# Kernel tuning notes

Hardware: AMD Instinct MI355X
Metric: run time of the kernel (lower is better)

The kernel has to match this reference:

```python
import jax, jax.numpy as jnp
import numpy as np

B, S, HS = 2, 2048, 2048
H, KVH, D = 8, 1, 256
ROPE_BASE = 10000.0


def _rope_cos_sin(position_ids, dim, base=ROPE_BASE):
    # position_ids: (B, S) int -> cos/sin: (B, S, dim)
    inv_freq = 1.0 / (base ** (jnp.arange(0, dim, 2, dtype=jnp.float32) / dim))
    thetas = position_ids.astype(jnp.float32)[..., None] * inv_freq  # (B,S,dim/2)
    emb = jnp.concatenate([thetas, thetas], axis=-1)  # (B,S,dim)
    return jnp.cos(emb), jnp.sin(emb)


def _rotate_half(x):
    x1, x2 = jnp.split(x, 2, axis=-1)
    return jnp.concatenate([-x2, x1], axis=-1)


def _apply_rope(q, k, cos, sin):
    # q,k: (B,h,S,D); cos,sin: (B,S,D) -> unsqueeze head dim
    cos = cos[:, None, :, :]
    sin = sin[:, None, :, :]
    q_emb = q * cos + _rotate_half(q) * sin
    k_emb = k * cos + _rotate_half(k) * sin
    return q_emb, k_emb


def setup_inputs() -> dict:
    key = jax.random.key(0)
    k0, k1, k2, k3, k4 = jax.random.split(key, 5)
    hidden_states = jax.random.normal(k0, (B, S, HS), jnp.float32)
    # causal additive mask: 0 where j<=i, large negative otherwise
    causal = jnp.tril(jnp.ones((S, S), dtype=bool))
    attention_mask = jnp.where(causal, 0.0, -1e9).astype(jnp.float32)
    attention_mask = jnp.broadcast_to(attention_mask[None, None], (B, 1, S, S))
    position_ids = jnp.broadcast_to(jnp.arange(S, dtype=jnp.int32)[None], (B, S))
    scale = 0.02
    Wq = jax.random.normal(k1, (HS, H * D), jnp.float32) * scale
    Wk = jax.random.normal(k2, (HS, KVH * D), jnp.float32) * scale
    Wv = jax.random.normal(k3, (HS, KVH * D), jnp.float32) * scale
    Wo = jax.random.normal(k4, (H * D, HS), jnp.float32) * scale
    return {"hidden_states": hidden_states, "attention_mask": attention_mask,
            "position_ids": position_ids, "Wq": Wq, "Wk": Wk, "Wv": Wv, "Wo": Wo}


def reference(hidden_states, attention_mask, position_ids, Wq, Wk, Wv, Wo):
    bs, seq_len, _ = hidden_states.shape
    q = (hidden_states @ Wq).reshape(bs, seq_len, H, D).transpose(0, 2, 1, 3)     # (B,H,S,D)
    k = (hidden_states @ Wk).reshape(bs, seq_len, KVH, D).transpose(0, 2, 1, 3)   # (B,KVH,S,D)
    v = (hidden_states @ Wv).reshape(bs, seq_len, KVH, D).transpose(0, 2, 1, 3)
    cos, sin = _rope_cos_sin(position_ids, D)
    q, k = _apply_rope(q, k, cos, sin)
    n_rep = H // KVH
    k = jnp.repeat(k, n_rep, axis=1)  # GQA repeat -> (B,H,S,D)
    v = jnp.repeat(v, n_rep, axis=1)
    scores = jnp.einsum('bhqd,bhkd->bhqk', q, k) / jnp.sqrt(jnp.float32(D))
    scores = scores + attention_mask
    attn = jax.nn.softmax(scores.astype(jnp.float32), axis=-1).astype(q.dtype)
    out = jnp.einsum('bhqk,bhkd->bhqd', attn, v)            # (B,H,S,D)
    out = out.transpose(0, 2, 1, 3).reshape(bs, seq_len, H * D)
    return out @ Wo
```

## Files before the change

kernel.cpp:

```cpp
#include <hip/hip_runtime.h>
#include <hip/hip_bf16.h>

typedef __bf16 bf16x8 __attribute__((ext_vector_type(8)));
typedef __bf16 bf16x4 __attribute__((ext_vector_type(4)));
typedef float  f32x4  __attribute__((ext_vector_type(4)));

#define MFMA16(a, b, c) __builtin_amdgcn_mfma_f32_16x16x32_bf16((a), (b), (c), 0, 0, 0)

#define GLOBAL_AS(p) ((const __attribute__((address_space(1))) void*)(p))
#define LDS_AS(p)    ((__attribute__((address_space(3))) void*)(p))

__global__ __launch_bounds__(256) void cvt_bf16_kernel(const float* __restrict__ in,
                                                       __bf16* __restrict__ out)
{
    const int idx = blockIdx.x * 256 + threadIdx.x;
    const float4* p = (const float4*)in + (size_t)idx * 2;
    float4 a = p[0], b = p[1];
    bf16x8 o;
    o[0] = (__bf16)a.x; o[1] = (__bf16)a.y; o[2] = (__bf16)a.z; o[3] = (__bf16)a.w;
    o[4] = (__bf16)b.x; o[5] = (__bf16)b.y; o[6] = (__bf16)b.z; o[7] = (__bf16)b.w;
    ((bf16x8*)out)[idx] = o;
}

__global__ __launch_bounds__(128) void trig_kernel(float2* __restrict__ cs)
{
    const int s = blockIdx.x, i = threadIdx.x;
    const float theta = (float)s * exp2f((float)i * (-13.287712379549449f / 128.f));
    float sn, c;
    sincosf(theta, &sn, &c);
    cs[s * 128 + i] = make_float2(c, sn);
}

__global__ __launch_bounds__(256) void transpose_cvt_kernel(const float* __restrict__ W,
                                                            __bf16* __restrict__ Bt,
                                                            int K, int N)
{
    __shared__ float t[32][33];
    const int n0 = blockIdx.x * 32, k0 = blockIdx.y * 32;
    const int x = threadIdx.x, y = threadIdx.y;
#pragma unroll
    for (int r = 0; r < 4; ++r)
        t[y + r * 8][x] = W[(size_t)(k0 + y + r * 8) * N + n0 + x];
    __syncthreads();
#pragma unroll
    for (int r = 0; r < 4; ++r)
        Bt[(size_t)(n0 + y + r * 8) * K + k0 + x] = (__bf16)t[x][y + r * 8];
}

__global__ __launch_bounds__(256) void vt_kernel(const __bf16* __restrict__ qkv,
                                                 __bf16* __restrict__ vT)
{
    __shared__ __bf16 t[32][33];
    const int s0 = blockIdx.x * 32, d0 = blockIdx.y * 32, b = blockIdx.z;
    const int x = threadIdx.x, y = threadIdx.y;
#pragma unroll
    for (int r = 0; r < 4; ++r)
        t[y + r * 8][x] = qkv[(size_t)(b * 2048 + s0 + y + r * 8) * 2560 + 2304 + d0 + x];
    __syncthreads();
#pragma unroll
    for (int r = 0; r < 4; ++r)
        vT[(size_t)(b * 256 + d0 + y + r * 8) * 2048 + s0 + x] = t[x][y + r * 8];
}

template <typename TC>
__global__ __launch_bounds__(256) void gemm_bt(const __bf16* __restrict__ A,
                                               const __bf16* __restrict__ Bt,
                                               TC* __restrict__ C,
                                               int M, int N, int K)
{
    __shared__ __bf16 As[128 * 32];
    __shared__ __bf16 Bs[128 * 32];

    const int tid  = threadIdx.x;
    const int wave = tid >> 6, lane = tid & 63;
    const int quad = lane >> 4, l16 = lane & 15;
    const int wm = (wave >> 1) * 64, wn = (wave & 1) * 64;
    const int bm = blockIdx.y * 128, bn = blockIdx.x * 128;

    f32x4 acc[4][4] = {};

    for (int k0 = 0; k0 < K; k0 += 32) {
        __syncthreads();
#pragma unroll
        for (int c = 0; c < 2; ++c) {
            const int off = tid * 16 + c * 4096;
            const int row = off >> 6;
            const int kb  = (off & 63) >> 1;
            const __bf16* ga = A  + (size_t)(bm + row) * K + k0 + kb;
            const __bf16* gb = Bt + (size_t)(bn + row) * K + k0 + kb;
            __builtin_amdgcn_global_load_lds(GLOBAL_AS(ga), LDS_AS(As + (off >> 1)), 16, 0, 0);
            __builtin_amdgcn_global_load_lds(GLOBAL_AS(gb), LDS_AS(Bs + (off >> 1)), 16, 0, 0);
        }
        __syncthreads();

        bf16x8 af[4];
#pragma unroll
        for (int mi = 0; mi < 4; ++mi)
            af[mi] = *(const bf16x8*)&As[(wm + mi * 16 + l16) * 32 + quad * 8];
#pragma unroll
        for (int ni = 0; ni < 4; ++ni) {
            bf16x8 bfr = *(const bf16x8*)&Bs[(wn + ni * 16 + l16) * 32 + quad * 8];
#pragma unroll
            for (int mi = 0; mi < 4; ++mi)
                acc[mi][ni] = MFMA16(af[mi], bfr, acc[mi][ni]);
        }
    }
#pragma unroll
    for (int mi = 0; mi < 4; ++mi)
#pragma unroll
        for (int ni = 0; ni < 4; ++ni)
#pragma unroll
            for (int r = 0; r < 4; ++r) {
                int row = bm + wm + mi * 16 + quad * 4 + r;
                int col = bn + wn + ni * 16 + l16;
                C[(size_t)row * N + col] = (TC)acc[mi][ni][r];
            }
}

__global__ __launch_bounds__(256) void rope_kernel(__bf16* __restrict__ qkv,
                                                   const float2* __restrict__ cs)
{
    const int bs = blockIdx.x;
    const int s = bs & 2047;
    const int t = threadIdx.x;
    const float QS = 0.09016843787599907f;

    const int hh = t >> 5, i0 = (t & 31) * 4;
    float2 c0 = cs[s * 128 + i0 + 0], c1 = cs[s * 128 + i0 + 1];
    float2 c2 = cs[s * 128 + i0 + 2], c3 = cs[s * 128 + i0 + 3];

    {
        __bf16* p = qkv + (size_t)bs * 2560 + hh * 256 + i0;
        bf16x4 x1 = *(const bf16x4*)p;
        bf16x4 x2 = *(const bf16x4*)(p + 128);
        bf16x4 o1, o2;
        o1[0] = (__bf16)(((float)x1[0] * c0.x - (float)x2[0] * c0.y) * QS);
        o2[0] = (__bf16)(((float)x2[0] * c0.x + (float)x1[0] * c0.y) * QS);
        o1[1] = (__bf16)(((float)x1[1] * c1.x - (float)x2[1] * c1.y) * QS);
        o2[1] = (__bf16)(((float)x2[1] * c1.x + (float)x1[1] * c1.y) * QS);
        o1[2] = (__bf16)(((float)x1[2] * c2.x - (float)x2[2] * c2.y) * QS);
        o2[2] = (__bf16)(((float)x2[2] * c2.x + (float)x1[2] * c2.y) * QS);
        o1[3] = (__bf16)(((float)x1[3] * c3.x - (float)x2[3] * c3.y) * QS);
        o2[3] = (__bf16)(((float)x2[3] * c3.x + (float)x1[3] * c3.y) * QS);
        *(bf16x4*)p = o1;
        *(bf16x4*)(p + 128) = o2;
    }
    if (t < 32) {
        const int j0 = t * 4;
        float2 d0 = cs[s * 128 + j0 + 0], d1 = cs[s * 128 + j0 + 1];
        float2 d2 = cs[s * 128 + j0 + 2], d3 = cs[s * 128 + j0 + 3];
        __bf16* p = qkv + (size_t)bs * 2560 + 2048 + j0;
        bf16x4 x1 = *(const bf16x4*)p;
        bf16x4 x2 = *(const bf16x4*)(p + 128);
        bf16x4 o1, o2;
        o1[0] = (__bf16)((float)x1[0] * d0.x - (float)x2[0] * d0.y);
        o2[0] = (__bf16)((float)x2[0] * d0.x + (float)x1[0] * d0.y);
        o1[1] = (__bf16)((float)x1[1] * d1.x - (float)x2[1] * d1.y);
        o2[1] = (__bf16)((float)x2[1] * d1.x + (float)x1[1] * d1.y);
        o1[2] = (__bf16)((float)x1[2] * d2.x - (float)x2[2] * d2.y);
        o2[2] = (__bf16)((float)x2[2] * d2.x + (float)x1[2] * d2.y);
        o1[3] = (__bf16)((float)x1[3] * d3.x - (float)x2[3] * d3.y);
        o2[3] = (__bf16)((float)x2[3] * d3.x + (float)x1[3] * d3.y);
        *(bf16x4*)p = o1;
        *(bf16x4*)(p + 128) = o2;
    }
}

__global__ __launch_bounds__(256) void attn_kernel(const __bf16* __restrict__ qkv,
                                                   const __bf16* __restrict__ vTg,
                                                   __bf16* __restrict__ og)
{
    __shared__ __bf16 Ks[64 * 256];
    __shared__ __bf16 Vs[256 * 64];
    __shared__ __bf16 Ps[4][16][68];

    const int b = blockIdx.z, h = blockIdx.y;
    const int xx = (int)blockIdx.x;
    const int half = xx >> 1;
    const bool rev = ((xx & 1) == 0) ^ (b != 0);
    const int qt = rev ? 31 - half : half;
    const int q0 = qt * 64;
    const int tid  = threadIdx.x;
    const int wave = tid >> 6, lane = tid & 63;
    const int quad = lane >> 4, l16 = lane & 15;
    const int xork = l16 & 7;

    bf16x8 onef;
#pragma unroll
    for (int e = 0; e < 8; ++e) onef[e] = (__bf16)1.0f;

    const int qrow = q0 + wave * 16 + l16;
    const __bf16* qptr = qkv + (size_t)(b * 2048 + qrow) * 2560 + h * 256;
    bf16x8 qf[8];
#pragma unroll
    for (int dc = 0; dc < 8; ++dc)
        qf[dc] = *(const bf16x8*)(qptr + dc * 32 + quad * 8);

    f32x4 oacc[17] = {};

    const int kKey0 = tid >> 5;
    const int kC    = (tid & 31) ^ (kKey0 & 7);
    const __bf16* kstage0 = qkv + (size_t)b * 2048 * 2560 + 2048
                          + (size_t)kKey0 * 2560 + kC * 8;
    const int vD0 = tid >> 3;
    const int vC  = (tid & 7) ^ (vD0 & 7);
    const __bf16* vstage0 = vTg + (size_t)b * 256 * 2048 + (size_t)vD0 * 2048 + vC * 8;

    int ckK[8];
#pragma unroll
    for (int dc = 0; dc < 8; ++dc) ckK[dc] = (dc * 4 + quad) ^ xork;
    const int chV0 = quad ^ xork;
    const int chV1 = (4 + quad) ^ xork;

    for (int j0 = 0; j0 <= q0; j0 += 64) {
        __syncthreads();
        const __bf16* kst = kstage0 + (size_t)j0 * 2560;
        const __bf16* vst = vstage0 + j0;
#pragma unroll
        for (int p = 0; p < 8; ++p)
            __builtin_amdgcn_global_load_lds(GLOBAL_AS(kst + (size_t)p * 8 * 2560),
                                             LDS_AS(Ks + tid * 8 + p * 2048), 16, 0, 0);
#pragma unroll
        for (int p = 0; p < 8; ++p)
            __builtin_amdgcn_global_load_lds(GLOBAL_AS(vst + (size_t)p * 32 * 2048),
                                             LDS_AS(Vs + tid * 8 + p * 2048), 16, 0, 0);
        __syncthreads();

        f32x4 sc[4] = {};
#pragma unroll
        for (int nt = 0; nt < 4; ++nt) {
            const __bf16* krow = &Ks[(nt * 16 + l16) * 256];
#pragma unroll
            for (int dc = 0; dc < 8; ++dc) {
                bf16x8 kf = *(const bf16x8*)(krow + ckK[dc] * 8);
                sc[nt] = MFMA16(qf[dc], kf, sc[nt]);
            }
        }
        if (j0 == q0) {
#pragma unroll
            for (int nt = 0; nt < 4; ++nt) {
                int key = j0 + nt * 16 + l16;
#pragma unroll
                for (int r = 0; r < 4; ++r) {
                    int row = q0 + wave * 16 + quad * 4 + r;
                    if (key > row) sc[nt][r] = -1e30f;
                }
            }
        }
#pragma unroll
        for (int nt = 0; nt < 4; ++nt)
#pragma unroll
            for (int r = 0; r < 4; ++r)
                Ps[wave][quad * 4 + r][nt * 16 + l16] = (__bf16)exp2f(sc[nt][r] - 8.f);
        bf16x8 pf0 = *(const bf16x8*)&Ps[wave][l16][quad * 8];
        bf16x8 pf1 = *(const bf16x8*)&Ps[wave][l16][32 + quad * 8];
#pragma unroll
        for (int dt = 0; dt < 16; ++dt) {
            const __bf16* vrow = &Vs[(dt * 16 + l16) * 64];
            bf16x8 vf0 = *(const bf16x8*)(vrow + chV0 * 8);
            bf16x8 vf1 = *(const bf16x8*)(vrow + chV1 * 8);
            oacc[dt] = MFMA16(pf0, vf0, oacc[dt]);
            oacc[dt] = MFMA16(pf1, vf1, oacc[dt]);
        }
        oacc[16] = MFMA16(pf0, onef, oacc[16]);
        oacc[16] = MFMA16(pf1, onef, oacc[16]);
    }
    float invl[4];
#pragma unroll
    for (int r = 0; r < 4; ++r) invl[r] = 1.f / oacc[16][r];
#pragma unroll
    for (int dt = 0; dt < 16; ++dt)
#pragma unroll
        for (int r = 0; r < 4; ++r) {
            int row = q0 + wave * 16 + quad * 4 + r;
            int col = h * 256 + dt * 16 + l16;
            og[(size_t)(b * 2048 + row) * 2048 + col] = (__bf16)(oacc[dt][r] * invl[r]);
        }
}

extern "C" void kernel_launch(void* const* d_in, const int* in_sizes, int n_in,
                              void* d_out, int out_size, void* d_ws, size_t ws_size,
                              hipStream_t stream)
{
    (void)in_sizes; (void)n_in; (void)out_size; (void)ws_size;
    const float* hidden = (const float*)d_in[0];
    const float* Wq = (const float*)d_in[3];
    const float* Wk = (const float*)d_in[4];
    const float* Wv = (const float*)d_in[5];
    const float* Wo = (const float*)d_in[6];

    char* ws = (char*)d_ws;
    __bf16* hb    = (__bf16*)(ws);
    __bf16* qkv   = (__bf16*)(ws + (16u << 20));
    __bf16* vTb   = (__bf16*)(ws + (36u << 20));
    __bf16* ob    = (__bf16*)(ws + (38u << 20));
    __bf16* Wqkvt = (__bf16*)(ws + (54u << 20));
    __bf16* Wot   = (__bf16*)(ws + (64u << 20));
    float2* csb   = (float2*)(ws + (72u << 20));
    float* out = (float*)d_out;

    dim3 blk(256);
    dim3 tblk(32, 8);
    cvt_bf16_kernel<<<dim3(4096), blk, 0, stream>>>(hidden, hb);
    trig_kernel<<<dim3(2048), dim3(128), 0, stream>>>(csb);
    transpose_cvt_kernel<<<dim3(64, 64), tblk, 0, stream>>>(Wq, Wqkvt, 2048, 2048);
    transpose_cvt_kernel<<<dim3(8, 64), tblk, 0, stream>>>(Wk, Wqkvt + (size_t)2048 * 2048, 2048, 256);
    transpose_cvt_kernel<<<dim3(8, 64), tblk, 0, stream>>>(Wv, Wqkvt + (size_t)2304 * 2048, 2048, 256);
    transpose_cvt_kernel<<<dim3(64, 64), tblk, 0, stream>>>(Wo, Wot, 2048, 2048);
    gemm_bt<__bf16><<<dim3(20, 32), blk, 0, stream>>>(hb, Wqkvt, qkv, 4096, 2560, 2048);
    rope_kernel<<<dim3(4096), blk, 0, stream>>>(qkv, csb);
    vt_kernel<<<dim3(64, 8, 2), tblk, 0, stream>>>(qkv, vTb);
    attn_kernel<<<dim3(32, 8, 2), blk, 0, stream>>>(qkv, vTb, ob);
    gemm_bt<float><<<dim3(16, 32), blk, 0, stream>>>(ob, Wot, out, 4096, 2048, 2048);
}
```

Before: 359.2 us.

## Double-buffer GEMM LDS tiles, widen to 128x256 blocks, XOR-swizzle LDS

The GEMM kernel now stages the next K-slice into a second LDS buffer while computing on the current one, with one barrier per iteration instead of two. Blocks grow to 512 threads covering a 128x256 output tile, which halves the number of blocks and reuses each A tile across more columns. LDS chunk placement is XOR-swizzled to reduce bank conflicts on fragment reads. In exchange, LDS use per block rises, and the grid shrinks to 320 and 256 blocks, which may underfill the GPU's compute units.

```diff
diff --git a/kernel.cpp b/kernel.cpp
--- a/kernel.cpp
+++ b/kernel.cpp
@@ -63,48 +63,66 @@
 }
 
 template <typename TC>
-__global__ __launch_bounds__(256) void gemm_bt(const __bf16* __restrict__ A,
-                                               const __bf16* __restrict__ Bt,
-                                               TC* __restrict__ C,
-                                               int M, int N, int K)
-{
-    __shared__ __bf16 As[128 * 32];
-    __shared__ __bf16 Bs[128 * 32];
+__global__ __launch_bounds__(512, 4) void gemm_bt(const __bf16* __restrict__ A,
+                                                  const __bf16* __restrict__ Bt,
+                                                  TC* __restrict__ C,
+                                                  int M, int N, int K)
+{
+    __shared__ __bf16 As[2][128 * 32];
+    __shared__ __bf16 Bs[2][256 * 32];
 
     const int tid  = threadIdx.x;
     const int wave = tid >> 6, lane = tid & 63;
     const int quad = lane >> 4, l16 = lane & 15;
-    const int wm = (wave >> 1) * 64, wn = (wave & 1) * 64;
-    const int bm = blockIdx.y * 128, bn = blockIdx.x * 128;
+    const int wm = (wave >> 2) * 64, wn = (wave & 3) * 64;
+    const int bm = blockIdx.y * 128, bn = blockIdx.x * 256;
+
+    const int srow    = tid >> 2;
+    const int schunk  = (tid & 3) ^ ((tid >> 3) & 3);
+    const __bf16* gA  = A  + (size_t)(bm + srow) * K + schunk * 8;
+    const __bf16* gB0 = Bt + (size_t)(bn + srow) * K + schunk * 8;
+    const __bf16* gB1 = Bt + (size_t)(bn + 128 + srow) * K + schunk * 8;
+    const int dstoff = tid * 16;
+    const int xorkey = (l16 >> 1) & 3;
 
     f32x4 acc[4][4] = {};
-
-    for (int k0 = 0; k0 < K; k0 += 32) {
-        __syncthreads();
-#pragma unroll
-        for (int c = 0; c < 2; ++c) {
-            const int off = tid * 16 + c * 4096;
-            const int row = off >> 6;
-            const int kb  = (off & 63) >> 1;
-            const __bf16* ga = A  + (size_t)(bm + row) * K + k0 + kb;
-            const __bf16* gb = Bt + (size_t)(bn + row) * K + k0 + kb;
-            __builtin_amdgcn_global_load_lds(GLOBAL_AS(ga), LDS_AS(As + (off >> 1)), 16, 0, 0);
-            __builtin_amdgcn_global_load_lds(GLOBAL_AS(gb), LDS_AS(Bs + (off >> 1)), 16, 0, 0);
-        }
-        __syncthreads();
-
+    const int nk = K >> 5;
+
+#define STAGE_G(buf, ks) do {                                                        \
+    const size_t koff = (size_t)(ks) * 32;                                           \
+    __builtin_amdgcn_global_load_lds(GLOBAL_AS(gA  + koff),                          \
+        LDS_AS((char*)As[buf] + dstoff), 16, 0, 0);                                  \
+    __builtin_amdgcn_global_load_lds(GLOBAL_AS(gB0 + koff),                          \
+        LDS_AS((char*)Bs[buf] + dstoff), 16, 0, 0);                                  \
+    __builtin_amdgcn_global_load_lds(GLOBAL_AS(gB1 + koff),                          \
+        LDS_AS((char*)Bs[buf] + 8192 + dstoff), 16, 0, 0);                           \
+} while (0)
+
+    STAGE_G(0, 0);
+    __syncthreads();
+
+    int cur = 0;
+    for (int ks = 0; ks < nk; ++ks) {
+        if (ks + 1 < nk) STAGE_G(cur ^ 1, ks + 1);
+
+        const __bf16* as = As[cur];
+        const __bf16* bs = Bs[cur];
         bf16x8 af[4];
 #pragma unroll
         for (int mi = 0; mi < 4; ++mi)
-            af[mi] = *(const bf16x8*)&As[(wm + mi * 16 + l16) * 32 + quad * 8];
+            af[mi] = *(const bf16x8*)&as[(wm + mi * 16 + l16) * 32 + (quad ^ xorkey) * 8];
 #pragma unroll
         for (int ni = 0; ni < 4; ++ni) {
-            bf16x8 bfr = *(const bf16x8*)&Bs[(wn + ni * 16 + l16) * 32 + quad * 8];
+            bf16x8 bfr = *(const bf16x8*)&bs[(wn + ni * 16 + l16) * 32 + (quad ^ xorkey) * 8];
 #pragma unroll
             for (int mi = 0; mi < 4; ++mi)
                 acc[mi][ni] = MFMA16(af[mi], bfr, acc[mi][ni]);
         }
+        __syncthreads();
+        cur ^= 1;
     }
+#undef STAGE_G
+
 #pragma unroll
     for (int mi = 0; mi < 4; ++mi)
 #pragma unroll
@@ -300,6 +318,7 @@
     float* out = (float*)d_out;
 
     dim3 blk(256);
+    dim3 gblk(512);
     dim3 tblk(32, 8);
     cvt_bf16_kernel<<<dim3(4096), blk, 0, stream>>>(hidden, hb);
     trig_kernel<<<dim3(2048), dim3(128), 0, stream>>>(csb);
@@ -307,9 +326,9 @@
     transpose_cvt_kernel<<<dim3(8, 64), tblk, 0, stream>>>(Wk, Wqkvt + (size_t)2048 * 2048, 2048, 256);
     transpose_cvt_kernel<<<dim3(8, 64), tblk, 0, stream>>>(Wv, Wqkvt + (size_t)2304 * 2048, 2048, 256);
     transpose_cvt_kernel<<<dim3(64, 64), tblk, 0, stream>>>(Wo, Wot, 2048, 2048);
-    gemm_bt<__bf16><<<dim3(20, 32), blk, 0, stream>>>(hb, Wqkvt, qkv, 4096, 2560, 2048);
+    gemm_bt<__bf16><<<dim3(10, 32), gblk, 0, stream>>>(hb, Wqkvt, qkv, 4096, 2560, 2048);
     rope_kernel<<<dim3(4096), blk, 0, stream>>>(qkv, csb);
     vt_kernel<<<dim3(64, 8, 2), tblk, 0, stream>>>(qkv, vTb);
     attn_kernel<<<dim3(32, 8, 2), blk, 0, stream>>>(qkv, vTb, ob);
-    gemm_bt<float><<<dim3(16, 32), blk, 0, stream>>>(ob, Wot, out, 4096, 2048, 2048);
-}
+    gemm_bt<float><<<dim3(8, 32), gblk, 0, stream>>>(ob, Wot, out, 4096, 2048, 2048);
+}
```

New measurement: 363.2 us. No clear change (+1.1%).

## Split attention waves 2x2 over query rows and key columns with LDS reduction

Applied to the files above, without the earlier changes.

The attention kernel changes its wave mapping from each wave owning 16 query rows across all 64 keys to a 2x2 grid. Each wave now owns 32 query rows and 32 keys of the tile, so each K and V fragment read from LDS feeds two MFMAs, halving per-wave LDS fragment traffic. Partial outputs and row sums from the two key-halves are combined through LDS scratch, reusing the Ks/Vs buffers, before the final normalisation and store. It also sets launch bounds to request two blocks per CU; with 64 accumulators per lane this risks register pressure or spills, and the extra reduction adds epilogue cost.

```diff
diff --git a/kernel.cpp b/kernel.cpp
--- a/kernel.cpp
+++ b/kernel.cpp
@@ -166,13 +166,13 @@
     }
 }
 
-__global__ __launch_bounds__(256) void attn_kernel(const __bf16* __restrict__ qkv,
-                                                   const __bf16* __restrict__ vTg,
-                                                   __bf16* __restrict__ og)
+__global__ __launch_bounds__(256, 2) void attn_kernel(const __bf16* __restrict__ qkv,
+                                                      const __bf16* __restrict__ vTg,
+                                                      __bf16* __restrict__ og)
 {
     __shared__ __bf16 Ks[64 * 256];
     __shared__ __bf16 Vs[256 * 64];
-    __shared__ __bf16 Ps[4][16][68];
+    __shared__ __bf16 Ps[4][32][36];
 
     const int b = blockIdx.z, h = blockIdx.y;
     const int xx = (int)blockIdx.x;
@@ -184,19 +184,24 @@
     const int wave = tid >> 6, lane = tid & 63;
     const int quad = lane >> 4, l16 = lane & 15;
     const int xork = l16 & 7;
+    const int wm2 = wave >> 1, wn2 = wave & 1;
 
     bf16x8 onef;
 #pragma unroll
     for (int e = 0; e < 8; ++e) onef[e] = (__bf16)1.0f;
 
-    const int qrow = q0 + wave * 16 + l16;
-    const __bf16* qptr = qkv + (size_t)(b * 2048 + qrow) * 2560 + h * 256;
-    bf16x8 qf[8];
-#pragma unroll
-    for (int dc = 0; dc < 8; ++dc)
-        qf[dc] = *(const bf16x8*)(qptr + dc * 32 + quad * 8);
-
-    f32x4 oacc[17] = {};
+    bf16x8 qf[2][8];
+#pragma unroll
+    for (int mi = 0; mi < 2; ++mi) {
+        const __bf16* qptr = qkv + (size_t)(b * 2048 + q0 + wm2 * 32 + mi * 16 + l16) * 2560
+                           + h * 256;
+#pragma unroll
+        for (int dc = 0; dc < 8; ++dc)
+            qf[mi][dc] = *(const bf16x8*)(qptr + dc * 32 + quad * 8);
+    }
+
+    f32x4 oacc[2][16] = {};
+    f32x4 lacc[2] = {};
 
     const int kKey0 = tid >> 5;
     const int kC    = (tid & 31) ^ (kKey0 & 7);
@@ -209,8 +214,7 @@
     int ckK[8];
 #pragma unroll
     for (int dc = 0; dc < 8; ++dc) ckK[dc] = (dc * 4 + quad) ^ xork;
-    const int chV0 = quad ^ xork;
-    const int chV1 = (4 + quad) ^ xork;
+    const int chV = (wn2 * 4 + quad) ^ xork;
 
     for (int j0 = 0; j0 <= q0; j0 += 64) {
         __syncthreads();
@@ -226,56 +230,88 @@
                                              LDS_AS(Vs + tid * 8 + p * 2048), 16, 0, 0);
         __syncthreads();
 
-        f32x4 sc[4] = {};
-#pragma unroll
-        for (int nt = 0; nt < 4; ++nt) {
-            const __bf16* krow = &Ks[(nt * 16 + l16) * 256];
+        f32x4 sc[2][2] = {};
+#pragma unroll
+        for (int nt = 0; nt < 2; ++nt) {
+            const __bf16* krow = &Ks[(wn2 * 32 + nt * 16 + l16) * 256];
 #pragma unroll
             for (int dc = 0; dc < 8; ++dc) {
                 bf16x8 kf = *(const bf16x8*)(krow + ckK[dc] * 8);
-                sc[nt] = MFMA16(qf[dc], kf, sc[nt]);
+                sc[0][nt] = MFMA16(qf[0][dc], kf, sc[0][nt]);
+                sc[1][nt] = MFMA16(qf[1][dc], kf, sc[1][nt]);
             }
         }
         if (j0 == q0) {
 #pragma unroll
-            for (int nt = 0; nt < 4; ++nt) {
-                int key = j0 + nt * 16 + l16;
-#pragma unroll
-                for (int r = 0; r < 4; ++r) {
-                    int row = q0 + wave * 16 + quad * 4 + r;
-                    if (key > row) sc[nt][r] = -1e30f;
-                }
+            for (int nt = 0; nt < 2; ++nt) {
+                int key = j0 + wn2 * 32 + nt * 16 + l16;
+#pragma unroll
+                for (int mi = 0; mi < 2; ++mi)
+#pragma unroll
+                    for (int r = 0; r < 4; ++r) {
+                        int row = q0 + wm2 * 32 + mi * 16 + quad * 4 + r;
+                        if (key > row) sc[mi][nt][r] = -1e30f;
+                    }
             }
         }
 #pragma unroll
-        for (int nt = 0; nt < 4; ++nt)
-#pragma unroll
-            for (int r = 0; r < 4; ++r)
-                Ps[wave][quad * 4 + r][nt * 16 + l16] = (__bf16)exp2f(sc[nt][r] - 8.f);
+        for (int mi = 0; mi < 2; ++mi)
+#pragma unroll
+            for (int nt = 0; nt < 2; ++nt)
+#pragma unroll
+                for (int r = 0; r < 4; ++r)
+                    Ps[wave][mi * 16 + quad * 4 + r][nt * 16 + l16] =
+                        (__bf16)exp2f(sc[mi][nt][r] - 8.f);
         bf16x8 pf0 = *(const bf16x8*)&Ps[wave][l16][quad * 8];
-        bf16x8 pf1 = *(const bf16x8*)&Ps[wave][l16][32 + quad * 8];
+        bf16x8 pf1 = *(const bf16x8*)&Ps[wave][16 + l16][quad * 8];
 #pragma unroll
         for (int dt = 0; dt < 16; ++dt) {
             const __bf16* vrow = &Vs[(dt * 16 + l16) * 64];
-            bf16x8 vf0 = *(const bf16x8*)(vrow + chV0 * 8);
-            bf16x8 vf1 = *(const bf16x8*)(vrow + chV1 * 8);
-            oacc[dt] = MFMA16(pf0, vf0, oacc[dt]);
-            oacc[dt] = MFMA16(pf1, vf1, oacc[dt]);
-        }
-        oacc[16] = MFMA16(pf0, onef, oacc[16]);
-        oacc[16] = MFMA16(pf1, onef, oacc[16]);
-    }
-    float invl[4];
-#pragma unroll
-    for (int r = 0; r < 4; ++r) invl[r] = 1.f / oacc[16][r];
-#pragma unroll
-    for (int dt = 0; dt < 16; ++dt)
-#pragma unroll
-        for (int r = 0; r < 4; ++r) {
-            int row = q0 + wave * 16 + quad * 4 + r;
-            int col = h * 256 + dt * 16 + l16;
-            og[(size_t)(b * 2048 + row) * 2048 + col] = (__bf16)(oacc[dt][r] * invl[r]);
-        }
+            bf16x8 vf = *(const bf16x8*)(vrow + chV * 8);
+            oacc[0][dt] = MFMA16(pf0, vf, oacc[0][dt]);
+            oacc[1][dt] = MFMA16(pf1, vf, oacc[1][dt]);
+        }
+        lacc[0] = MFMA16(pf0, onef, lacc[0]);
+        lacc[1] = MFMA16(pf1, onef, lacc[1]);
+    }
+
+    __syncthreads();
+    float* oscr = (wm2 == 0) ? (float*)Ks : (float*)Vs;
+    float* lscr = (float*)Ps;
+    if (wn2 == 1) {
+#pragma unroll
+        for (int mi = 0; mi < 2; ++mi) {
+#pragma unroll
+            for (int dt = 0; dt < 16; ++dt)
+#pragma unroll
+                for (int r = 0; r < 4; ++r)
+                    oscr[(mi * 16 + quad * 4 + r) * 256 + dt * 16 + l16] = oacc[mi][dt][r];
+#pragma unroll
+            for (int r = 0; r < 4; ++r)
+                lscr[(wm2 * 32 + mi * 16 + quad * 4 + r) * 16 + l16] = lacc[mi][r];
+        }
+    }
+    __syncthreads();
+    if (wn2 == 0) {
+#pragma unroll
+        for (int mi = 0; mi < 2; ++mi) {
+            float invl[4];
+#pragma unroll
+            for (int r = 0; r < 4; ++r)
+                invl[r] = 1.f / (lacc[mi][r]
+                        + lscr[(wm2 * 32 + mi * 16 + quad * 4 + r) * 16 + l16]);
+#pragma unroll
+            for (int dt = 0; dt < 16; ++dt)
+#pragma unroll
+                for (int r = 0; r < 4; ++r) {
+                    float o = oacc[mi][dt][r]
+                            + oscr[(mi * 16 + quad * 4 + r) * 256 + dt * 16 + l16];
+                    int row = q0 + wm2 * 32 + mi * 16 + quad * 4 + r;
+                    int col = h * 256 + dt * 16 + l16;
+                    og[(size_t)(b * 2048 + row) * 2048 + col] = (__bf16)(o * invl[r]);
+                }
+        }
+    }
 }
 
 extern "C" void kernel_launch(void* const* d_in, const int* in_sizes, int n_in,
```

New measurement: 357.9 us. About the same (-0.3%).

## Split attention key tiles across wave pairs with LDS reduction and MFMA priority

Applied to the files above, without the earlier changes.

The attention block grows from 4 to 8 waves. Each pair of waves shares a 16-row query slab and splits every 64-key tile into two 32-key halves, so each wave runs half the QK and PV MFMAs. The two partial output and row-sum accumulators are combined through LDS (reusing the K/V buffers) at the end. s_setprio is raised around the MFMA sections. This is meant to give more waves per CU for latency hiding and to halve per-wave accumulator registers, at the cost of an extra reduction pass and barrier, and Q fragments loaded twice.

```diff
diff --git a/kernel.cpp b/kernel.cpp
--- a/kernel.cpp
+++ b/kernel.cpp
@@ -166,13 +166,13 @@
     }
 }
 
-__global__ __launch_bounds__(256) void attn_kernel(const __bf16* __restrict__ qkv,
-                                                   const __bf16* __restrict__ vTg,
-                                                   __bf16* __restrict__ og)
+__global__ __launch_bounds__(512, 4) void attn_kernel(const __bf16* __restrict__ qkv,
+                                                      const __bf16* __restrict__ vTg,
+                                                      __bf16* __restrict__ og)
 {
     __shared__ __bf16 Ks[64 * 256];
     __shared__ __bf16 Vs[256 * 64];
-    __shared__ __bf16 Ps[4][16][68];
+    __shared__ __bf16 Ps[8][16][36];
 
     const int b = blockIdx.z, h = blockIdx.y;
     const int xx = (int)blockIdx.x;
@@ -184,19 +184,20 @@
     const int wave = tid >> 6, lane = tid & 63;
     const int quad = lane >> 4, l16 = lane & 15;
     const int xork = l16 & 7;
+    const int wq = wave >> 1, wk = wave & 1;
 
     bf16x8 onef;
 #pragma unroll
     for (int e = 0; e < 8; ++e) onef[e] = (__bf16)1.0f;
 
-    const int qrow = q0 + wave * 16 + l16;
-    const __bf16* qptr = qkv + (size_t)(b * 2048 + qrow) * 2560 + h * 256;
+    const __bf16* qptr = qkv + (size_t)(b * 2048 + q0 + wq * 16 + l16) * 2560 + h * 256;
     bf16x8 qf[8];
 #pragma unroll
     for (int dc = 0; dc < 8; ++dc)
         qf[dc] = *(const bf16x8*)(qptr + dc * 32 + quad * 8);
 
-    f32x4 oacc[17] = {};
+    f32x4 oacc[16] = {};
+    f32x4 lacc = {};
 
     const int kKey0 = tid >> 5;
     const int kC    = (tid & 31) ^ (kKey0 & 7);
@@ -209,73 +210,92 @@
     int ckK[8];
 #pragma unroll
     for (int dc = 0; dc < 8; ++dc) ckK[dc] = (dc * 4 + quad) ^ xork;
-    const int chV0 = quad ^ xork;
-    const int chV1 = (4 + quad) ^ xork;
+    const int chV = (wk * 4 + quad) ^ xork;
 
     for (int j0 = 0; j0 <= q0; j0 += 64) {
         __syncthreads();
         const __bf16* kst = kstage0 + (size_t)j0 * 2560;
         const __bf16* vst = vstage0 + j0;
 #pragma unroll
-        for (int p = 0; p < 8; ++p)
-            __builtin_amdgcn_global_load_lds(GLOBAL_AS(kst + (size_t)p * 8 * 2560),
-                                             LDS_AS(Ks + tid * 8 + p * 2048), 16, 0, 0);
-#pragma unroll
-        for (int p = 0; p < 8; ++p)
-            __builtin_amdgcn_global_load_lds(GLOBAL_AS(vst + (size_t)p * 32 * 2048),
-                                             LDS_AS(Vs + tid * 8 + p * 2048), 16, 0, 0);
+        for (int p = 0; p < 4; ++p)
+            __builtin_amdgcn_global_load_lds(GLOBAL_AS(kst + (size_t)p * 16 * 2560),
+                                             LDS_AS(Ks + tid * 8 + p * 4096), 16, 0, 0);
+#pragma unroll
+        for (int p = 0; p < 4; ++p)
+            __builtin_amdgcn_global_load_lds(GLOBAL_AS(vst + (size_t)p * 64 * 2048),
+                                             LDS_AS(Vs + tid * 8 + p * 4096), 16, 0, 0);
         __syncthreads();
 
-        f32x4 sc[4] = {};
-#pragma unroll
-        for (int nt = 0; nt < 4; ++nt) {
-            const __bf16* krow = &Ks[(nt * 16 + l16) * 256];
+        f32x4 sc[2] = {};
+        __builtin_amdgcn_s_setprio(1);
+#pragma unroll
+        for (int nt = 0; nt < 2; ++nt) {
+            const __bf16* krow = &Ks[(wk * 32 + nt * 16 + l16) * 256];
 #pragma unroll
             for (int dc = 0; dc < 8; ++dc) {
                 bf16x8 kf = *(const bf16x8*)(krow + ckK[dc] * 8);
                 sc[nt] = MFMA16(qf[dc], kf, sc[nt]);
             }
         }
+        __builtin_amdgcn_s_setprio(0);
         if (j0 == q0) {
 #pragma unroll
-            for (int nt = 0; nt < 4; ++nt) {
-                int key = j0 + nt * 16 + l16;
+            for (int nt = 0; nt < 2; ++nt) {
+                int key = j0 + wk * 32 + nt * 16 + l16;
 #pragma unroll
                 for (int r = 0; r < 4; ++r) {
-                    int row = q0 + wave * 16 + quad * 4 + r;
+                    int row = q0 + wq * 16 + quad * 4 + r;
                     if (key > row) sc[nt][r] = -1e30f;
                 }
             }
         }
 #pragma unroll
-        for (int nt = 0; nt < 4; ++nt)
+        for (int nt = 0; nt < 2; ++nt)
 #pragma unroll
             for (int r = 0; r < 4; ++r)
                 Ps[wave][quad * 4 + r][nt * 16 + l16] = (__bf16)exp2f(sc[nt][r] - 8.f);
-        bf16x8 pf0 = *(const bf16x8*)&Ps[wave][l16][quad * 8];
-        bf16x8 pf1 = *(const bf16x8*)&Ps[wave][l16][32 + quad * 8];
+        bf16x8 pf = *(const bf16x8*)&Ps[wave][l16][quad * 8];
+        __builtin_amdgcn_s_setprio(1);
 #pragma unroll
         for (int dt = 0; dt < 16; ++dt) {
             const __bf16* vrow = &Vs[(dt * 16 + l16) * 64];
-            bf16x8 vf0 = *(const bf16x8*)(vrow + chV0 * 8);
-            bf16x8 vf1 = *(const bf16x8*)(vrow + chV1 * 8);
-            oacc[dt] = MFMA16(pf0, vf0, oacc[dt]);
-            oacc[dt] = MFMA16(pf1, vf1, oacc[dt]);
-        }
-        oacc[16] = MFMA16(pf0, onef, oacc[16]);
-        oacc[16] = MFMA16(pf1, onef, oacc[16]);
-    }
-    float invl[4];
-#pragma unroll
-    for (int r = 0; r < 4; ++r) invl[r] = 1.f / oacc[16][r];
-#pragma unroll
-    for (int dt = 0; dt < 16; ++dt)
-#pragma unroll
-        for (int r = 0; r < 4; ++r) {
-            int row = q0 + wave * 16 + quad * 4 + r;
-            int col = h * 256 + dt * 16 + l16;
-            og[(size_t)(b * 2048 + row) * 2048 + col] = (__bf16)(oacc[dt][r] * invl[r]);
-        }
+            bf16x8 vf = *(const bf16x8*)(vrow + chV * 8);
+            oacc[dt] = MFMA16(pf, vf, oacc[dt]);
+        }
+        lacc = MFMA16(pf, onef, lacc);
+        __builtin_amdgcn_s_setprio(0);
+    }
+
+    __syncthreads();
+    float* oscr = (wq < 2) ? ((float*)Ks + wq * 4096)
+                           : ((float*)Vs + (wq - 2) * 4096);
+    float* lscr = (float*)Ps;
+    if (wk == 1) {
+#pragma unroll
+        for (int dt = 0; dt < 16; ++dt)
+#pragma unroll
+            for (int r = 0; r < 4; ++r)
+                oscr[(quad * 4 + r) * 256 + dt * 16 + l16] = oacc[dt][r];
+#pragma unroll
+        for (int r = 0; r < 4; ++r)
+            lscr[(wq * 16 + quad * 4 + r) * 16 + l16] = lacc[r];
+    }
+    __syncthreads();
+    if (wk == 0) {
+        float invl[4];
+#pragma unroll
+        for (int r = 0; r < 4; ++r)
+            invl[r] = 1.f / (lacc[r] + lscr[(wq * 16 + quad * 4 + r) * 16 + l16]);
+#pragma unroll
+        for (int dt = 0; dt < 16; ++dt)
+#pragma unroll
+            for (int r = 0; r < 4; ++r) {
+                float o = oacc[dt][r] + oscr[(quad * 4 + r) * 256 + dt * 16 + l16];
+                int row = q0 + wq * 16 + quad * 4 + r;
+                int col = h * 256 + dt * 16 + l16;
+                og[(size_t)(b * 2048 + row) * 2048 + col] = (__bf16)(o * invl[r]);
+            }
+    }
 }
 
 extern "C" void kernel_launch(void* const* d_in, const int* in_sizes, int n_in,
@@ -310,6 +330,6 @@
     gemm_bt<__bf16><<<dim3(20, 32), blk, 0, stream>>>(hb, Wqkvt, qkv, 4096, 2560, 2048);
     rope_kernel<<<dim3(4096), blk, 0, stream>>>(qkv, csb);
     vt_kernel<<<dim3(64, 8, 2), tblk, 0, stream>>>(qkv, vTb);
-    attn_kernel<<<dim3(32, 8, 2), blk, 0, stream>>>(qkv, vTb, ob);
+    attn_kernel<<<dim3(32, 8, 2), dim3(512), 0, stream>>>(qkv, vTb, ob);
     gemm_bt<float><<<dim3(16, 32), blk, 0, stream>>>(ob, Wot, out, 4096, 2048, 2048);
 }
```

Measured after the change: 365.1 us. No clear change (+1.6%).
